# Kernel tuning notes

Measured on AMD Instinct MI355X. Metric: run time of the kernel, lower is better.

Reference implementation:

```python
import jax, jax.numpy as jnp
import numpy as np
from jax import lax

B, R, C_FEAT, HF, WF = 4, 512, 256, 50, 50
NUM_CLASSES = 91
POOL = 7
SCALE = 1.0 / 16.0
IMG_H = IMG_W = 800.0
SCORE_THRESH = 0.05
NMS_THRESH = 0.5
DETS_PER_IMG = 100
TOPK_NMS = 2048  # fixed-size candidate set for static-shape NMS
BBOX_W = np.array([10.0, 10.0, 5.0, 5.0], np.float32)
BBOX_CLIP = float(np.log(1000.0 / 16.0))
MIN_SIZE = 0.01


def setup_inputs():
    key = jax.random.key(0)
    ks = jax.random.split(key, 8)
    features = jax.random.normal(ks[0], (B, C_FEAT, HF, WF), jnp.float32)
    cxy = jax.random.uniform(ks[1], (B, R, 2), jnp.float32, 50.0, 750.0)
    wh = jax.random.uniform(ks[2], (B, R, 2), jnp.float32, 20.0, 200.0)
    proposals = jnp.concatenate([cxy - wh / 2, cxy + wh / 2], axis=-1)
    d_in = C_FEAT * POOL * POOL
    def lin(k, fi, fo):
        return jax.random.normal(k, (fi, fo), jnp.float32) / np.sqrt(fi)
    return {
        'features': features, 'proposals': proposals,
        'W1': lin(ks[3], d_in, 1024), 'b1': jnp.zeros((1024,), jnp.float32),
        'W2': lin(ks[4], 1024, 1024), 'b2': jnp.zeros((1024,), jnp.float32),
        'Wc': lin(ks[5], 1024, NUM_CLASSES), 'bc': jnp.zeros((NUM_CLASSES,), jnp.float32),
        'Wr': lin(ks[6], 1024, 4 * NUM_CLASSES), 'br': jnp.zeros((4 * NUM_CLASSES,), jnp.float32),
    }


def roi_align(features, proposals):
    # features [B,C,H,W], proposals [B,R,4] in image coords -> [B*R, C*POOL*POOL]
    featT = jnp.transpose(features, (0, 2, 3, 1))  # [B,H,W,C]
    boxes = proposals * SCALE
    x1, y1, x2, y2 = (boxes[..., i] for i in range(4))
    bh = (y2 - y1) / POOL
    bw = (x2 - x1) / POOL
    centers = jnp.arange(POOL, dtype=jnp.float32) + 0.5
    ys = y1[..., None] + centers * bh[..., None]  # [B,R,P]
    xs = x1[..., None] + centers * bw[..., None]  # [B,R,P]

    def bil(fT, ys_b, xs_b):  # per-image bilinear sampling
        yy = jnp.broadcast_to(ys_b[:, :, None], (R, POOL, POOL))
        xx = jnp.broadcast_to(xs_b[:, None, :], (R, POOL, POOL))
        y = jnp.clip(yy, 0.0, HF - 1.0)
        x = jnp.clip(xx, 0.0, WF - 1.0)
        y0 = jnp.floor(y); x0 = jnp.floor(x)
        y0i = y0.astype(jnp.int32); x0i = x0.astype(jnp.int32)
        y1i = jnp.minimum(y0i + 1, HF - 1); x1i = jnp.minimum(x0i + 1, WF - 1)
        ly = y - y0; lx = x - x0; hy = 1.0 - ly; hx = 1.0 - lx
        f00 = fT[y0i, x0i]; f01 = fT[y0i, x1i]
        f10 = fT[y1i, x0i]; f11 = fT[y1i, x1i]  # [R,P,P,C]
        out = ((hy * hx)[..., None] * f00 + (hy * lx)[..., None] * f01 +
               (ly * hx)[..., None] * f10 + (ly * lx)[..., None] * f11)
        return out  # [R,P,P,C]

    pooled = jax.vmap(bil)(featT, ys, xs)  # [B,R,P,P,C]
    pooled = jnp.transpose(pooled, (0, 1, 4, 2, 3))  # [B,R,C,P,P] (torch layout)
    return pooled.reshape(B * R, -1)


def decode_boxes(box_reg, props):
    # box_reg [N, 4*NC], props [N,4] -> [N,NC,4]
    w = props[:, 2] - props[:, 0]
    h = props[:, 3] - props[:, 1]
    cx = props[:, 0] + 0.5 * w
    cy = props[:, 1] + 0.5 * h
    d = box_reg.reshape(-1, NUM_CLASSES, 4) / jnp.asarray(BBOX_W)
    dx, dy = d[..., 0], d[..., 1]
    dw = jnp.minimum(d[..., 2], BBOX_CLIP)
    dh = jnp.minimum(d[..., 3], BBOX_CLIP)
    pcx = dx * w[:, None] + cx[:, None]
    pcy = dy * h[:, None] + cy[:, None]
    pw = jnp.exp(dw) * w[:, None]
    ph = jnp.exp(dh) * h[:, None]
    return jnp.stack([pcx - 0.5 * pw, pcy - 0.5 * ph,
                      pcx + 0.5 * pw, pcy + 0.5 * ph], axis=-1)


def box_iou(a, b):
    area_a = (a[:, 2] - a[:, 0]) * (a[:, 3] - a[:, 1])
    area_b = (b[:, 2] - b[:, 0]) * (b[:, 3] - b[:, 1])
    lt = jnp.maximum(a[:, None, :2], b[None, :, :2])
    rb = jnp.minimum(a[:, None, 2:], b[None, :, 2:])
    wh = jnp.clip(rb - lt, 0.0)
    inter = wh[..., 0] * wh[..., 1]
    return inter / (area_a[:, None] + area_b[None, :] - inter)


def post_image(boxes, scores):
    # boxes [R,NC,4], scores [R,NC] -> fixed-size top DETS_PER_IMG detections
    x1 = jnp.clip(boxes[..., 0], 0.0, IMG_W)
    y1 = jnp.clip(boxes[..., 1], 0.0, IMG_H)
    x2 = jnp.clip(boxes[..., 2], 0.0, IMG_W)
    y2 = jnp.clip(boxes[..., 3], 0.0, IMG_H)
    boxes = jnp.stack([x1, y1, x2, y2], axis=-1)
    # drop background class 0, flatten (roi, class) candidates
    boxes = boxes[:, 1:].reshape(-1, 4)            # [R*(NC-1),4]
    scores = scores[:, 1:].reshape(-1)
    labels = jnp.broadcast_to(jnp.arange(1, NUM_CLASSES, dtype=jnp.int32)[None, :],
                              (R, NUM_CLASSES - 1)).reshape(-1)
    wv = boxes[:, 2] - boxes[:, 0]
    hv = boxes[:, 3] - boxes[:, 1]
    valid = (scores > SCORE_THRESH) & (wv >= MIN_SIZE) & (hv >= MIN_SIZE)
    cand = jnp.where(valid, scores, -1.0)
    top_s, top_i = lax.top_k(cand, TOPK_NMS)       # sorted desc by score
    b_k = boxes[top_i]
    l_k = labels[top_i]
    v_k = valid[top_i]
    # batched (per-class) NMS via label offset
    off = l_k.astype(jnp.float32)[:, None] * (IMG_W + 1.0)
    iou = box_iou(b_k + off, b_k + off)            # [K,K]
    idx = jnp.arange(TOPK_NMS)

    def body(i, keep):
        sup = jnp.any((idx < i) & keep & (iou[:, i] > NMS_THRESH))
        return keep.at[i].set(keep[i] & ~sup)

    keep = lax.fori_loop(0, TOPK_NMS, body, v_k)
    fs = jnp.where(keep, top_s, -1.0)
    out_s, out_i = lax.top_k(fs, DETS_PER_IMG)
    ok = out_s > 0.0
    out_b = jnp.where(ok[:, None], b_k[out_i], 0.0)
    out_l = jnp.where(ok, l_k[out_i], 0)
    out_s = jnp.where(ok, out_s, 0.0)
    return out_b, out_s, out_l


def reference(features, proposals, W1, b1, W2, b2, Wc, bc, Wr, br):
    x = roi_align(features, proposals)               # [B*R, C*49]
    x = jax.nn.relu(x @ W1 + b1)
    x = jax.nn.relu(x @ W2 + b2)
    class_logits = x @ Wc + bc                        # [B*R, NC]
    box_regression = x @ Wr + br                      # [B*R, 4*NC]
    props_flat = proposals.reshape(-1, 4)
    pred_boxes = decode_boxes(box_regression, props_flat).reshape(B, R, NUM_CLASSES, 4)
    pred_scores = jax.nn.softmax(class_logits, axis=-1).reshape(B, R, NUM_CLASSES)
    boxes, scores, labels = jax.vmap(post_image)(pred_boxes, pred_scores)
    return boxes, scores, labels


if __name__ == '__main__':
    out = reference(**setup_inputs())
    print([o.shape for o in out])
```

## Files before the change

### kernel.cpp

```cpp
#include <hip/hip_runtime.h>
#include <stdint.h>

#define NBI 4
#define RRI 512
#define NROI 2048
#define DIN 12544
#define BBOX_CLIP_F 4.135166556742356f

typedef _Float16 half8 __attribute__((ext_vector_type(8)));
typedef float f32x16 __attribute__((ext_vector_type(16)));

#define GLDS(g, l)                                                                   \
  __builtin_amdgcn_global_load_lds((const __attribute__((address_space(1))) void*)(g), \
                                   (__attribute__((address_space(3))) void*)(l), 16, 0, 0)

#define O_AH      10240000ull
#define O_AL      61620224ull
#define O_WTH     113000448ull
#define O_WTL     138690560ull
#define OZ        164380672ull
#define WS_NEED   189546496ull

#define O_X2H     0ull
#define O_X2L     2097152ull
#define O_X1H     O_AH
#define O_X1L     (O_AH + 4194304ull)
#define O_PBOX    O_AL
#define O_KEYS    (O_AL + 2949120ull)
#define O_NMSBOX  (O_AL + 3473408ull)
#define O_OUTBOX  (O_AL + 3604480ull)
#define O_SCORE   (O_AL + 3735552ull)
#define O_LABEL   (O_AL + 3768320ull)
#define O_CNT     (O_AL + 3801088ull)
#define O_MASK    (O_AL + 3802112ull)
#define O_WHH     O_WTH
#define O_WHL     (O_WTH + 1048576ull)
#define O_BH      (O_WTH + 2097152ull)
#define O_PARTH   (O_WTH + 2101248ull)
#define O_W2TH    OZ
#define O_W2TL    (OZ + 2097152ull)
#define O_PFC2    (OZ + 4194304ull)

__global__ __launch_bounds__(256) void k_transpose(const float* __restrict__ f,
                                                   float* __restrict__ ft,
                                                   float* __restrict__ out) {
  __shared__ float s[32][33];
  int b = blockIdx.z;
  int hw0 = blockIdx.x << 5;
  int c0 = blockIdx.y << 5;
  if (blockIdx.y == 0 && blockIdx.z == 0 && blockIdx.x < 10) {
    int i = blockIdx.x * 256 + threadIdx.x;
    if (i < 2400) out[i] = 0.0f;
  }
  int tx = threadIdx.x & 31, ty = threadIdx.x >> 5;
#pragma unroll
  for (int j = 0; j < 32; j += 8) {
    int hw = hw0 + tx;
    if (hw < 2500) s[ty + j][tx] = f[((size_t)b * 256 + c0 + ty + j) * 2500 + hw];
  }
  __syncthreads();
#pragma unroll
  for (int j = 0; j < 32; j += 8) {
    int hw = hw0 + ty + j;
    if (hw < 2500) ft[((size_t)b * 2500 + hw) * 256 + c0 + tx] = s[tx][ty + j];
  }
}

__global__ __launch_bounds__(256) void k_wsplit(const float* __restrict__ W,
                                                _Float16* __restrict__ Th,
                                                _Float16* __restrict__ Tl, int K, int N) {
  __shared__ float s[64][68];
  int k0 = blockIdx.x << 6, n0 = blockIdx.y << 6;
  int t = threadIdx.x;
  int r = t >> 2, c4 = (t & 3) << 4;
#pragma unroll
  for (int j = 0; j < 16; j += 4) {
    float4 v = *(const float4*)(W + (size_t)(k0 + r) * N + n0 + c4 + j);
    s[r][c4 + j] = v.x; s[r][c4 + j + 1] = v.y; s[r][c4 + j + 2] = v.z; s[r][c4 + j + 3] = v.w;
  }
  __syncthreads();
  int nr = t >> 2, kc = (t & 3) << 4;
  half8 h8[2], l8[2];
#pragma unroll
  for (int j = 0; j < 16; ++j) {
    float v = s[kc + j][nr];
    _Float16 h = (_Float16)v;
    _Float16 lo = (_Float16)((v - (float)h) * 2048.0f);
    h8[j >> 3][j & 7] = h;
    l8[j >> 3][j & 7] = lo;
  }
  size_t base = (size_t)(n0 + nr) * K + k0 + kc;
  *(half8*)(Th + base) = h8[0]; *(half8*)(Th + base + 8) = h8[1];
  *(half8*)(Tl + base) = l8[0]; *(half8*)(Tl + base + 8) = l8[1];
}

__global__ __launch_bounds__(256) void k_prep2(const float* __restrict__ W2,
                                               const float* __restrict__ Wc,
                                               const float* __restrict__ Wr,
                                               const float* __restrict__ bcv,
                                               const float* __restrict__ brv,
                                               _Float16* __restrict__ T2h,
                                               _Float16* __restrict__ T2l,
                                               _Float16* __restrict__ Th,
                                               _Float16* __restrict__ Tl,
                                               float* __restrict__ bh,
                                               unsigned* __restrict__ keys32,
                                               unsigned* __restrict__ cnt) {
  int blk = blockIdx.x;
  int t = threadIdx.x;
  if (blk < 256) {
    __shared__ float s[64][68];
    int k0 = (blk & 15) << 6, n0 = (blk >> 4) << 6;
    int r = t >> 2, c4 = (t & 3) << 4;
#pragma unroll
    for (int j = 0; j < 16; j += 4) {
      float4 v = *(const float4*)(W2 + (size_t)(k0 + r) * 1024 + n0 + c4 + j);
      s[r][c4 + j] = v.x; s[r][c4 + j + 1] = v.y; s[r][c4 + j + 2] = v.z; s[r][c4 + j + 3] = v.w;
    }
    __syncthreads();
    int nr = t >> 2, kc = (t & 3) << 4;
    half8 h8[2], l8[2];
#pragma unroll
    for (int j = 0; j < 16; ++j) {
      float v = s[kc + j][nr];
      _Float16 h = (_Float16)v;
      _Float16 lo = (_Float16)((v - (float)h) * 2048.0f);
      h8[j >> 3][j & 7] = h;
      l8[j >> 3][j & 7] = lo;
    }
    size_t base = (size_t)(n0 + nr) * 1024 + k0 + kc;
    *(half8*)(T2h + base) = h8[0]; *(half8*)(T2h + base + 8) = h8[1];
    *(half8*)(T2l + base) = l8[0]; *(half8*)(T2l + base + 8) = l8[1];
  } else {
    int n = blk - 256;
    keys32[(n << 8) + t] = 0u;
    if (n == 0 && t < 64) cnt[t] = 0u;
    for (int k = t; k < 1024; k += 256) {
      float v = (n < 91) ? Wc[(size_t)k * 91 + n]
                         : ((n < 455) ? Wr[(size_t)k * 364 + (n - 91)] : 0.0f);
      _Float16 h = (_Float16)v;
      Th[(size_t)n * 1024 + k] = h;
      Tl[(size_t)n * 1024 + k] = (_Float16)((v - (float)h) * 2048.0f);
    }
    if (t == 0) bh[n] = (n < 91) ? bcv[n] : ((n < 455) ? brv[n - 91] : 0.0f);
  }
}

__global__ __launch_bounds__(256) void k_roialign(const float* __restrict__ ft,
                                                  const float* __restrict__ props,
                                                  _Float16* __restrict__ Ahg,
                                                  _Float16* __restrict__ Alg) {
  __shared__ float pool[DIN];
  __shared__ float lyA[7], lxA[7];
  __shared__ int y0A[7], y1A[7], x0A[7], x1A[7];
  int roi = blockIdx.x;
  int b = roi >> 9;
  const float* p = props + (size_t)roi * 4;
  float x1s = p[0] * 0.0625f, y1s = p[1] * 0.0625f;
  float x2s = p[2] * 0.0625f, y2s = p[3] * 0.0625f;
  float bh = (y2s - y1s) / 7.0f;
  float bw = (x2s - x1s) / 7.0f;
  int t = threadIdx.x;
  if (t < 7) {
    float y = y1s + ((float)t + 0.5f) * bh;
    y = fminf(fmaxf(y, 0.0f), 49.0f);
    float y0 = floorf(y);
    int y0i = (int)y0;
    y0A[t] = y0i; y1A[t] = min(y0i + 1, 49); lyA[t] = y - y0;
  } else if (t < 14) {
    int px = t - 7;
    float x = x1s + ((float)px + 0.5f) * bw;
    x = fminf(fmaxf(x, 0.0f), 49.0f);
    float x0 = floorf(x);
    int x0i = (int)x0;
    x0A[px] = x0i; x1A[px] = min(x0i + 1, 49); lxA[px] = x - x0;
  }
  __syncthreads();
  const float* fb = ft + (size_t)b * 2500 * 256;
  int c = t;
  for (int p49 = 0; p49 < 49; ++p49) {
    int py = p49 / 7, px = p49 - py * 7;
    int y0 = y0A[py], y1 = y1A[py], x0 = x0A[px], x1 = x1A[px];
    float ly = lyA[py], lx = lxA[px], hy = 1.0f - ly, hx = 1.0f - lx;
    float f00 = fb[(y0 * 50 + x0) * 256 + c];
    float f01 = fb[(y0 * 50 + x1) * 256 + c];
    float f10 = fb[(y1 * 50 + x0) * 256 + c];
    float f11 = fb[(y1 * 50 + x1) * 256 + c];
    pool[c * 49 + p49] = (hy * hx) * f00 + (hy * lx) * f01 + (ly * hx) * f10 + (ly * lx) * f11;
  }
  __syncthreads();
  _Float16* dh = Ahg + (size_t)roi * DIN;
  _Float16* dl = Alg + (size_t)roi * DIN;
  for (int i8 = t; i8 < 1568; i8 += 256) {
    half8 h8v, l8v;
#pragma unroll
    for (int j = 0; j < 8; ++j) {
      float v = pool[i8 * 8 + j];
      _Float16 h = (_Float16)v;
      h8v[j] = h;
      l8v[j] = (_Float16)((v - (float)h) * 2048.0f);
    }
    *(half8*)(dh + (size_t)i8 * 8) = h8v;
    *(half8*)(dl + (size_t)i8 * 8) = l8v;
  }
}

__global__ __launch_bounds__(256, 2) void k_mfma(const _Float16* __restrict__ Ah,
                                                 const _Float16* __restrict__ Al,
                                                 const _Float16* __restrict__ Bh,
                                                 const _Float16* __restrict__ Bl,
                                                 float* __restrict__ P0,
                                                 float* __restrict__ P2,
                                                 int K, int K2, int ldc, int MN) {
  __shared__ __align__(16) half8 sA[2][2][512];
  __shared__ __align__(16) half8 sB[2][2][512];
  int gx = gridDim.x, gy = gridDim.y;
  int nwg = gx * gy * gridDim.z;
  int lin = blockIdx.x + gx * (blockIdx.y + gy * blockIdx.z);
  int cpx = nwg >> 3;
  int nl = (lin & 7) * cpx + (lin >> 3);
  int sx = __ffs(gx) - 1, sy = __ffs(gy) - 1;
  int lx = nl & (gx - 1);
  int rest = nl >> sx;
  int ly = rest & (gy - 1);
  int lz = rest >> sy;
  int m0 = ly << 7, n0 = lx << 7;
  int kb = lz * K2;
  int t = threadIdx.x;
  int w = t >> 6, l = t & 63;
  int wr = w >> 1, wc = w & 1;
  int fr = l & 31, cgrp = l >> 5;
  int rowA = m0 + 32 * w + (l & 31);
  int rowB = n0 + 32 * w + (l & 31);
  int kc0 = (l >> 5) << 3;
  const _Float16* gAh = Ah + (size_t)rowA * K + kb + kc0;
  const _Float16* gAl = Al + (size_t)rowA * K + kb + kc0;
  const _Float16* gBh = Bh + (size_t)rowB * K + kb + kc0;
  const _Float16* gBl = Bl + (size_t)rowB * K + kb + kc0;
  int sh0 = 128 * w, sh1 = 128 * w + 64;
  int sa0 = wr * 256 + cgrp * 32 + fr;
  int sb0 = wc * 256 + cgrp * 32 + fr;
  f32x16 accH[2][2], accL[2][2];
#pragma unroll
  for (int i = 0; i < 2; ++i)
#pragma unroll
    for (int j = 0; j < 2; ++j)
#pragma unroll
      for (int r = 0; r < 16; ++r) { accH[i][j][r] = 0.0f; accL[i][j][r] = 0.0f; }
  GLDS(gAh, &sA[0][0][sh0]); GLDS(gAh + 16, &sA[0][0][sh1]);
  GLDS(gAl, &sA[0][1][sh0]); GLDS(gAl + 16, &sA[0][1][sh1]);
  GLDS(gBh, &sB[0][0][sh0]); GLDS(gBh + 16, &sB[0][0][sh1]);
  GLDS(gBl, &sB[0][1][sh0]); GLDS(gBl + 16, &sB[0][1][sh1]);
  __syncthreads();
  for (int kt = 0; kt < K2; kt += 32) {
    int buf = (kt >> 5) & 1;
    int nb = buf ^ 1;
    bool more = (kt + 32) < K2;
    if (more) {
      int o = kt + 32;
      GLDS(gAh + o, &sA[nb][0][sh0]); GLDS(gAh + o + 16, &sA[nb][0][sh1]);
      GLDS(gAl + o, &sA[nb][1][sh0]); GLDS(gAl + o + 16, &sA[nb][1][sh1]);
      GLDS(gBh + o, &sB[nb][0][sh0]); GLDS(gBh + o + 16, &sB[nb][0][sh1]);
      GLDS(gBl + o, &sB[nb][1][sh0]); GLDS(gBl + o + 16, &sB[nb][1][sh1]);
    }
#pragma unroll
    for (int s = 0; s < 2; ++s) {
      half8 aH[2], aL[2], bH[2], bL[2];
#pragma unroll
      for (int mf = 0; mf < 2; ++mf) {
        int sa = sa0 + mf * 128 + s * 64;
        aH[mf] = sA[buf][0][sa];
        aL[mf] = sA[buf][1][sa];
      }
#pragma unroll
      for (int nf = 0; nf < 2; ++nf) {
        int sb = sb0 + nf * 128 + s * 64;
        bH[nf] = sB[buf][0][sb];
        bL[nf] = sB[buf][1][sb];
      }
#pragma unroll
      for (int mf = 0; mf < 2; ++mf)
#pragma unroll
        for (int nf = 0; nf < 2; ++nf) {
          accH[mf][nf] =
              __builtin_amdgcn_mfma_f32_32x32x16_f16(aH[mf], bH[nf], accH[mf][nf], 0, 0, 0);
          accL[mf][nf] =
              __builtin_amdgcn_mfma_f32_32x32x16_f16(aH[mf], bL[nf], accL[mf][nf], 0, 0, 0);
          accL[mf][nf] =
              __builtin_amdgcn_mfma_f32_32x32x16_f16(aL[mf], bH[nf], accL[mf][nf], 0, 0, 0);
        }
    }
    if (more) __syncthreads();
  }
  float* Pz = (lz == 2) ? P2 : (P0 + (size_t)(lz == 3 ? 2 : lz) * MN);
  const float sc = 4.8828125e-4f;
#pragma unroll
  for (int mf = 0; mf < 2; ++mf)
#pragma unroll
    for (int nf = 0; nf < 2; ++nf) {
      int col = n0 + wc * 64 + nf * 32 + fr;
      int rbase = m0 + wr * 64 + mf * 32 + 4 * cgrp;
#pragma unroll
      for (int r = 0; r < 16; ++r) {
        int row = rbase + (r & 3) + ((r >> 2) << 3);
        Pz[(size_t)row * ldc + col] = accH[mf][nf][r] + accL[mf][nf][r] * sc;
      }
    }
}

__global__ void k_reduce_split(const float* __restrict__ P0, const float* __restrict__ P2,
                               const float* __restrict__ bias, _Float16* __restrict__ xh,
                               _Float16* __restrict__ xl, int S) {
  const int MN = 2048 * 1024;
  int i8 = blockIdx.x * 256 + threadIdx.x;
  size_t base = (size_t)i8 * 8;
  float v[8];
  {
    float4 a0 = *(const float4*)(P0 + base);
    float4 a1 = *(const float4*)(P0 + base + 4);
    float4 b0 = *(const float4*)(P0 + MN + base);
    float4 b1 = *(const float4*)(P0 + MN + base + 4);
    v[0] = a0.x + b0.x; v[1] = a0.y + b0.y; v[2] = a0.z + b0.z; v[3] = a0.w + b0.w;
    v[4] = a1.x + b1.x; v[5] = a1.y + b1.y; v[6] = a1.z + b1.z; v[7] = a1.w + b1.w;
  }
  if (S == 4) {
    float4 c0 = *(const float4*)(P2 + base);
    float4 c1 = *(const float4*)(P2 + base + 4);
    float4 d0 = *(const float4*)(P0 + 2 * (size_t)MN + base);
    float4 d1 = *(const float4*)(P0 + 2 * (size_t)MN + base + 4);
    v[0] = (v[0] + c0.x) + d0.x; v[1] = (v[1] + c0.y) + d0.y;
    v[2] = (v[2] + c0.z) + d0.z; v[3] = (v[3] + c0.w) + d0.w;
    v[4] = (v[4] + c1.x) + d1.x; v[5] = (v[5] + c1.y) + d1.y;
    v[6] = (v[6] + c1.z) + d1.z; v[7] = (v[7] + c1.w) + d1.w;
  }
  int cb = (int)(base & 1023);
  float4 b0 = *(const float4*)(bias + cb);
  float4 b1v = *(const float4*)(bias + cb + 4);
  v[0] += b0.x; v[1] += b0.y; v[2] += b0.z; v[3] += b0.w;
  v[4] += b1v.x; v[5] += b1v.y; v[6] += b1v.z; v[7] += b1v.w;
  half8 h8, l8;
#pragma unroll
  for (int j = 0; j < 8; ++j) {
    float x = fmaxf(v[j], 0.0f);
    _Float16 h = (_Float16)x;
    h8[j] = h;
    l8[j] = (_Float16)((x - (float)h) * 2048.0f);
  }
  *(half8*)(xh + base) = h8;
  *(half8*)(xl + base) = l8;
}

__global__ __launch_bounds__(256) void k_softmax_decode(const float* __restrict__ PH,
                                                        const float* __restrict__ bh,
                                                        const float* __restrict__ props,
                                                        float* __restrict__ pbox,
                                                        unsigned long long* __restrict__ keys,
                                                        unsigned* __restrict__ cnt) {
  const int MNh = 2048 * 512;
  int wave = threadIdx.x >> 6, lane = threadIdx.x & 63;
  int roi = (blockIdx.x << 2) + wave;
  size_t eb = (size_t)roi * 512;
#define HREAD(e) ((((PH[(e)] + PH[(e) + MNh]) + PH[(e) + 3 * (size_t)MNh]) + \
                   PH[(e) + 2 * (size_t)MNh]) + bh[(e) - eb])
  float l0 = HREAD(eb + lane);
  float l1 = (lane < 27) ? HREAD(eb + lane + 64) : -3.4e38f;
  float m = fmaxf(l0, l1);
#pragma unroll
  for (int off = 32; off; off >>= 1) m = fmaxf(m, __shfl_xor(m, off));
  float e0 = expf(l0 - m);
  float e1 = (lane < 27) ? expf(l1 - m) : 0.0f;
  float ssum = e0 + e1;
#pragma unroll
  for (int off = 32; off; off >>= 1) ssum += __shfl_xor(ssum, off);
  const float* pr = props + (size_t)roi * 4;
  float w = pr[2] - pr[0], h = pr[3] - pr[1];
  float cx = pr[0] + 0.5f * w, cy = pr[1] + 0.5f * h;
  int img = roi >> 9, rl = roi & 511;
#pragma unroll
  for (int half = 0; half < 2; ++half) {
    int c = lane + half * 64;
    float e = half ? e1 : e0;
    if (c >= 1 && c <= 90) {
      float score = e / ssum;
      size_t rg = eb + 91 + (c << 2);
      float dx = HREAD(rg + 0) / 10.0f, dy = HREAD(rg + 1) / 10.0f;
      float dw = fminf(HREAD(rg + 2) / 5.0f, BBOX_CLIP_F);
      float dh = fminf(HREAD(rg + 3) / 5.0f, BBOX_CLIP_F);
      float pcx = dx * w + cx, pcy = dy * h + cy;
      float pw = expf(dw) * w, ph = expf(dh) * h;
      float bx1 = pcx - 0.5f * pw, by1 = pcy - 0.5f * ph;
      float bx2 = pcx + 0.5f * pw, by2 = pcy + 0.5f * ph;
      bx1 = fminf(fmaxf(bx1, 0.0f), 800.0f);
      by1 = fminf(fmaxf(by1, 0.0f), 800.0f);
      bx2 = fminf(fmaxf(bx2, 0.0f), 800.0f);
      by2 = fminf(fmaxf(by2, 0.0f), 800.0f);
      float* pb = pbox + ((size_t)roi * 90 + (c - 1)) * 4;
      pb[0] = bx1; pb[1] = by1; pb[2] = bx2; pb[3] = by2;
      if (score > 0.05f && (bx2 - bx1) >= 0.01f && (by2 - by1) >= 0.01f) {
        unsigned pos = atomicAdd(cnt + img, 1u);
        unsigned idx = (unsigned)rl * 90u + (unsigned)(c - 1);
        unsigned su = __float_as_uint(score);
        su ^= (su >> 31) ? 0xFFFFFFFFu : 0x80000000u;
        keys[((size_t)img << 14) + pos] =
            ((unsigned long long)su << 32) | (unsigned long long)(0xFFFFFFFFu - idx);
      }
    }
  }
#undef HREAD
}

__global__ void k_sort(unsigned long long* __restrict__ keys, const unsigned* __restrict__ cnt) {
  extern __shared__ unsigned long long s[];
  int img = blockIdx.x, tid = threadIdx.x;
  unsigned long long* kb = keys + ((size_t)img << 14);
  unsigned n = cnt[img];
  unsigned np = 2048; while (np < n && np < 16384) np <<= 1;
  if (np <= 8192) {
    for (unsigned i = tid; i < np; i += 1024) s[i] = kb[i];
    __syncthreads();
    for (unsigned k = 2; k <= np; k <<= 1) {
      for (unsigned j = k >> 1; j; j >>= 1) {
        for (unsigned x = tid; x < (np >> 1); x += 1024) {
          unsigned i = ((x & ~(j - 1)) << 1) | (x & (j - 1));
          unsigned l = i | j;
          bool up = ((i & k) == 0);
          unsigned long long a = s[i], b = s[l];
          if ((a > b) == up) { s[i] = b; s[l] = a; }
        }
        __syncthreads();
      }
    }
    for (unsigned i = tid; i < np; i += 1024) kb[i] = s[i];
  } else {
    for (int ch = 0; ch < 2; ++ch) {
      unsigned base = (unsigned)ch << 13;
      for (unsigned i = tid; i < 8192; i += 1024) s[i] = kb[base + i];
      __syncthreads();
      for (unsigned k = 2; k <= 8192; k <<= 1) {
        for (unsigned j = k >> 1; j; j >>= 1) {
          for (unsigned x = tid; x < 4096; x += 1024) {
            unsigned i = ((x & ~(j - 1)) << 1) | (x & (j - 1));
            unsigned l = i | j;
            bool up = (((base + i) & k) == 0);
            unsigned long long a = s[i], b = s[l];
            if ((a > b) == up) { s[i] = b; s[l] = a; }
          }
          __syncthreads();
        }
      }
      for (unsigned i = tid; i < 8192; i += 1024) kb[base + i] = s[i];
      __syncthreads();
    }
    for (unsigned x = tid; x < 8192; x += 1024) {
      unsigned long long a = kb[x], b = kb[x + 8192];
      if (a > b) { kb[x] = b; kb[x + 8192] = a; }
    }
    __syncthreads();
    for (int ch = 0; ch < 2; ++ch) {
      unsigned base = (unsigned)ch << 13;
      for (unsigned i = tid; i < 8192; i += 1024) s[i] = kb[base + i];
      __syncthreads();
      for (unsigned j = 4096; j; j >>= 1) {
        for (unsigned x = tid; x < 4096; x += 1024) {
          unsigned i = ((x & ~(j - 1)) << 1) | (x & (j - 1));
          unsigned l = i | j;
          unsigned long long a = s[i], b = s[l];
          if (a > b) { s[i] = b; s[l] = a; }
        }
        __syncthreads();
      }
      for (unsigned i = tid; i < 8192; i += 1024) kb[base + i] = s[i];
      __syncthreads();
    }
  }
}

__global__ void k_gather(const unsigned long long* __restrict__ keys,
                         const unsigned* __restrict__ cnt, const float* __restrict__ pbox,
                         float4* __restrict__ nmsbox, float4* __restrict__ outbox,
                         float* __restrict__ score, float* __restrict__ label) {
  int g = blockIdx.x * 256 + threadIdx.x;
  int img = g >> 11, slot = g & 2047;
  unsigned n = cnt[img];
  unsigned neff = n > 2048u ? 2048u : n;
  unsigned np = 2048; while (np < n && np < 16384) np <<= 1;
  float4 bo = make_float4(0, 0, 0, 0), bx = make_float4(0, 0, 0, 0);
  float sc = -1.0f, lb = 0.0f;
  if ((unsigned)slot < neff) {
    unsigned long long key = keys[((size_t)img << 14) + (np - 1 - slot)];
    unsigned su = (unsigned)(key >> 32);
    su = (su & 0x80000000u) ? (su ^ 0x80000000u) : ~su;
    sc = __uint_as_float(su);
    unsigned idx = 0xFFFFFFFFu - (unsigned)(key & 0xFFFFFFFFull);
    unsigned rl = idx / 90u, c = idx - rl * 90u;
    const float* pb = pbox + ((size_t)((img << 9) + rl) * 90 + c) * 4;
    bx = *(const float4*)pb;
    float off = (float)(c + 1) * 801.0f;
    bo = make_float4(bx.x + off, bx.y + off, bx.z + off, bx.w + off);
    lb = (float)(c + 1);
  }
  nmsbox[g] = bo; outbox[g] = bx; score[g] = sc; label[g] = lb;
}

__global__ __launch_bounds__(256) void k_mask(const float* __restrict__ nmsbox,
                                              unsigned* __restrict__ mask) {
  __shared__ float bx[2048 * 4];
  int img = blockIdx.x >> 9;
  int i0 = (blockIdx.x & 511) << 2;
  const float4* src = (const float4*)(nmsbox + (size_t)img * 2048 * 4);
  for (int q = threadIdx.x; q < 2048; q += 256) ((float4*)bx)[q] = src[q];
  __syncthreads();
  int w = threadIdx.x & 63, ir = threadIdx.x >> 6;
  int i = i0 + ir;
  float ax1 = bx[i * 4], ay1 = bx[i * 4 + 1], ax2 = bx[i * 4 + 2], ay2 = bx[i * 4 + 3];
  float areaA = (ax2 - ax1) * (ay2 - ay1);
  unsigned bits = 0;
  for (int jj = 0; jj < 32; ++jj) {
    int j2 = (jj + w) & 31;
    int j = (w << 5) + j2;
    float b1 = bx[j * 4], b2 = bx[j * 4 + 1], b3 = bx[j * 4 + 2], b4 = bx[j * 4 + 3];
    float areaB = (b3 - b1) * (b4 - b2);
    float lx = fmaxf(ax1, b1), lyv = fmaxf(ay1, b2);
    float rx = fminf(ax2, b3), ry = fminf(ay2, b4);
    float iw = fmaxf(rx - lx, 0.0f), ih = fmaxf(ry - lyv, 0.0f);
    float inter = iw * ih;
    float iou = inter / (areaA + areaB - inter);
    if (iou > 0.5f) bits |= (1u << j2);
  }
  mask[((size_t)img * 2048 + i) * 64 + w] = bits;
}

__global__ void k_scan(const unsigned* __restrict__ mask, const unsigned* __restrict__ cnt,
                       const float* __restrict__ outbox, const float* __restrict__ score,
                       const float* __restrict__ label, float* __restrict__ dout) {
  int img = blockIdx.x, lane = threadIdx.x;
  unsigned n = cnt[img];
  unsigned neff = n > 2048u ? 2048u : n;
  unsigned base = (unsigned)lane * 32u;
  unsigned rem;
  if (base + 32u <= neff) rem = 0u;
  else if (base >= neff) rem = 0xFFFFFFFFu;
  else rem = ~((1u << (neff - base)) - 1u);
  const unsigned* mrow = mask + (size_t)img * 2048 * 64;
  unsigned row = (neff > 0) ? mrow[lane] : 0u;
  int outc = 0;
  for (int i = 0; i < (int)neff; ++i) {
    unsigned nextrow = (i + 1 < (int)neff) ? mrow[(size_t)(i + 1) * 64 + lane] : 0u;
    unsigned wrd = __shfl(rem, i >> 5);
    bool kept = ((wrd >> (i & 31)) & 1u) == 0u;
    if (kept) {
      rem |= row;
      if (lane < 4)
        dout[(size_t)(img * 100 + outc) * 4 + lane] = outbox[((size_t)img * 2048 + i) * 4 + lane];
      if (lane == 0) {
        dout[1600 + img * 100 + outc] = score[img * 2048 + i];
        dout[2000 + img * 100 + outc] = label[img * 2048 + i];
      }
      ++outc;
      if (outc >= 100) break;
    }
    row = nextrow;
  }
}

extern "C" void kernel_launch(void* const* d_in, const int* in_sizes, int n_in,
                              void* d_out, int out_size, void* d_ws, size_t ws_size,
                              hipStream_t stream) {
  if (ws_size < WS_NEED) return;

  const float* features  = (const float*)d_in[0];
  const float* proposals = (const float*)d_in[1];
  const float* W1 = (const float*)d_in[2];
  const float* b1 = (const float*)d_in[3];
  const float* W2 = (const float*)d_in[4];
  const float* b2 = (const float*)d_in[5];
  const float* Wc = (const float*)d_in[6];
  const float* bc = (const float*)d_in[7];
  const float* Wr = (const float*)d_in[8];
  const float* br = (const float*)d_in[9];
  float* out = (float*)d_out;
  char* ws = (char*)d_ws;

  float* featT = (float*)(ws + 0);
  _Float16* Ahg = (_Float16*)(ws + O_AH);
  _Float16* Alg = (_Float16*)(ws + O_AL);
  _Float16* Wth = (_Float16*)(ws + O_WTH);
  _Float16* Wtl = (_Float16*)(ws + O_WTL);
  float* partZ = (float*)(ws + OZ);
  float* partF = (float*)(ws + 0);
  _Float16* x1h = (_Float16*)(ws + O_X1H);
  _Float16* x1l = (_Float16*)(ws + O_X1L);
  _Float16* W2th = (_Float16*)(ws + O_W2TH);
  _Float16* W2tl = (_Float16*)(ws + O_W2TL);
  float* partC = (float*)(ws + O_PFC2);
  _Float16* x2h = (_Float16*)(ws + O_X2H);
  _Float16* x2l = (_Float16*)(ws + O_X2L);
  _Float16* whh = (_Float16*)(ws + O_WHH);
  _Float16* whl = (_Float16*)(ws + O_WHL);
  float* bhv   = (float*)(ws + O_BH);
  float* partH = (float*)(ws + O_PARTH);
  float* partH2 = (float*)(ws + O_PARTH + 3ull * 4194304ull);
  float* pbox  = (float*)(ws + O_PBOX);
  unsigned long long* keys = (unsigned long long*)(ws + O_KEYS);
  float* nmsbox = (float*)(ws + O_NMSBOX);
  float* outbox = (float*)(ws + O_OUTBOX);
  float* scorea = (float*)(ws + O_SCORE);
  float* labela = (float*)(ws + O_LABEL);
  unsigned* cnt = (unsigned*)(ws + O_CNT);
  unsigned* maska = (unsigned*)(ws + O_MASK);

  k_transpose<<<dim3(79, 8, 4), 256, 0, stream>>>(features, featT, out);
  k_wsplit<<<dim3(196, 16), 256, 0, stream>>>(W1, Wth, Wtl, 12544, 1024);
  k_roialign<<<2048, 256, 0, stream>>>(featT, proposals, Ahg, Alg);
  k_mfma<<<dim3(8, 16, 4), 256, 0, stream>>>(Ahg, Alg, Wth, Wtl, partZ, partF,
                                             12544, 3136, 1024, 2048 * 1024);
  k_reduce_split<<<1024, 256, 0, stream>>>(partZ, partF, b1, x1h, x1l, 4);
  k_prep2<<<768, 256, 0, stream>>>(W2, Wc, Wr, bc, br, W2th, W2tl, whh, whl, bhv,
                                   (unsigned*)keys, cnt);
  k_mfma<<<dim3(8, 16, 2), 256, 0, stream>>>(x1h, x1l, W2th, W2tl, partC, partC,
                                             1024, 512, 1024, 2048 * 1024);
  k_reduce_split<<<1024, 256, 0, stream>>>(partC, partC, b2, x2h, x2l, 2);
  k_mfma<<<dim3(4, 16, 4), 256, 0, stream>>>(x2h, x2l, whh, whl, partH, partH2,
                                             1024, 256, 512, 2048 * 512);
  k_softmax_decode<<<512, 256, 0, stream>>>(partH, bhv, proposals, pbox, keys, cnt);
  k_sort<<<4, 1024, 65536, stream>>>(keys, cnt);
  k_gather<<<32, 256, 0, stream>>>(keys, cnt, pbox, (float4*)nmsbox, (float4*)outbox,
                                   scorea, labela);
  k_mask<<<2048, 256, 0, stream>>>(nmsbox, maska);
  k_scan<<<4, 64, 0, stream>>>(maska, cnt, outbox, scorea, labela, out);
}
```

Measured before the change: 395.2 us.

## Replace global_load_lds with register-staged prefetch into LDS double buffer

The GEMM tile loader moves from direct global-to-LDS async loads to ordinary vector global loads held in registers, prefetched two k-steps ahead and written to the alternate LDS buffer. Each thread now loads a contiguous 32-element half of a row, so global access coalescing and the LDS write pattern both change. The goal is better latency hiding and wider per-thread loads. The cost is more VGPR pressure, which can lower occupancy, plus explicit LDS store instructions.

Result: faster. 367.5 us (median of 2 runs) (-7.0%).

```diff
diff --git a/kernel.cpp b/kernel.cpp
--- a/kernel.cpp
+++ b/kernel.cpp
@@ -9,10 +9,6 @@
 
 typedef _Float16 half8 __attribute__((ext_vector_type(8)));
 typedef float f32x16 __attribute__((ext_vector_type(16)));
-
-#define GLDS(g, l)                                                                   \
-  __builtin_amdgcn_global_load_lds((const __attribute__((address_space(1))) void*)(g), \
-                                   (__attribute__((address_space(3))) void*)(l), 16, 0, 0)
 
 #define O_AH      10240000ull
 #define O_AL      61620224ull
@@ -230,14 +226,13 @@
   int w = t >> 6, l = t & 63;
   int wr = w >> 1, wc = w & 1;
   int fr = l & 31, cgrp = l >> 5;
-  int rowA = m0 + 32 * w + (l & 31);
-  int rowB = n0 + 32 * w + (l & 31);
-  int kc0 = (l >> 5) << 3;
-  const _Float16* gAh = Ah + (size_t)rowA * K + kb + kc0;
-  const _Float16* gAl = Al + (size_t)rowA * K + kb + kc0;
-  const _Float16* gBh = Bh + (size_t)rowB * K + kb + kc0;
-  const _Float16* gBl = Bl + (size_t)rowB * K + kb + kc0;
-  int sh0 = 128 * w, sh1 = 128 * w + 64;
+  int sr = t >> 1, sh = t & 1;
+  const _Float16* gAh = Ah + (size_t)(m0 + sr) * K + kb + sh * 16;
+  const _Float16* gAl = Al + (size_t)(m0 + sr) * K + kb + sh * 16;
+  const _Float16* gBh = Bh + (size_t)(n0 + sr) * K + kb + sh * 16;
+  const _Float16* gBl = Bl + (size_t)(n0 + sr) * K + kb + sh * 16;
+  int ws0 = ((sr >> 5) * 4 + 2 * sh) * 32 + (sr & 31);
+  int ws1 = ws0 + 32;
   int sa0 = wr * 256 + cgrp * 32 + fr;
   int sb0 = wc * 256 + cgrp * 32 + fr;
   f32x16 accH[2][2], accL[2][2];
@@ -247,21 +242,35 @@
     for (int j = 0; j < 2; ++j)
 #pragma unroll
       for (int r = 0; r < 16; ++r) { accH[i][j][r] = 0.0f; accL[i][j][r] = 0.0f; }
-  GLDS(gAh, &sA[0][0][sh0]); GLDS(gAh + 16, &sA[0][0][sh1]);
-  GLDS(gAl, &sA[0][1][sh0]); GLDS(gAl + 16, &sA[0][1][sh1]);
-  GLDS(gBh, &sB[0][0][sh0]); GLDS(gBh + 16, &sB[0][0][sh1]);
-  GLDS(gBl, &sB[0][1][sh0]); GLDS(gBl + 16, &sB[0][1][sh1]);
+  half8 rAh0 = *(const half8*)gAh, rAh1 = *(const half8*)(gAh + 8);
+  half8 rAl0 = *(const half8*)gAl, rAl1 = *(const half8*)(gAl + 8);
+  half8 rBh0 = *(const half8*)gBh, rBh1 = *(const half8*)(gBh + 8);
+  half8 rBl0 = *(const half8*)gBl, rBl1 = *(const half8*)(gBl + 8);
+  sA[0][0][ws0] = rAh0; sA[0][0][ws1] = rAh1;
+  sA[0][1][ws0] = rAl0; sA[0][1][ws1] = rAl1;
+  sB[0][0][ws0] = rBh0; sB[0][0][ws1] = rBh1;
+  sB[0][1][ws0] = rBl0; sB[0][1][ws1] = rBl1;
+  if (32 < K2) {
+    rAh0 = *(const half8*)(gAh + 32); rAh1 = *(const half8*)(gAh + 40);
+    rAl0 = *(const half8*)(gAl + 32); rAl1 = *(const half8*)(gAl + 40);
+    rBh0 = *(const half8*)(gBh + 32); rBh1 = *(const half8*)(gBh + 40);
+    rBl0 = *(const half8*)(gBl + 32); rBl1 = *(const half8*)(gBl + 40);
+  }
   __syncthreads();
   for (int kt = 0; kt < K2; kt += 32) {
     int buf = (kt >> 5) & 1;
-    int nb = buf ^ 1;
     bool more = (kt + 32) < K2;
     if (more) {
-      int o = kt + 32;
-      GLDS(gAh + o, &sA[nb][0][sh0]); GLDS(gAh + o + 16, &sA[nb][0][sh1]);
-      GLDS(gAl + o, &sA[nb][1][sh0]); GLDS(gAl + o + 16, &sA[nb][1][sh1]);
-      GLDS(gBh + o, &sB[nb][0][sh0]); GLDS(gBh + o + 16, &sB[nb][0][sh1]);
-      GLDS(gBl + o, &sB[nb][1][sh0]); GLDS(gBl + o + 16, &sB[nb][1][sh1]);
+      sA[buf ^ 1][0][ws0] = rAh0; sA[buf ^ 1][0][ws1] = rAh1;
+      sA[buf ^ 1][1][ws0] = rAl0; sA[buf ^ 1][1][ws1] = rAl1;
+      sB[buf ^ 1][0][ws0] = rBh0; sB[buf ^ 1][0][ws1] = rBh1;
+      sB[buf ^ 1][1][ws0] = rBl0; sB[buf ^ 1][1][ws1] = rBl1;
+    }
+    if ((kt + 64) < K2) {
+      rAh0 = *(const half8*)(gAh + kt + 64); rAh1 = *(const half8*)(gAh + kt + 72);
+      rAl0 = *(const half8*)(gAl + kt + 64); rAl1 = *(const half8*)(gAl + kt + 72);
+      rBh0 = *(const half8*)(gBh + kt + 64); rBh1 = *(const half8*)(gBh + kt + 72);
+      rBl0 = *(const half8*)(gBl + kt + 64); rBl1 = *(const half8*)(gBl + kt + 72);
     }
 #pragma unroll
     for (int s = 0; s < 2; ++s) {
```
